# Performance work log

Hardware: AMD Instinct MI355X
Metric: run time of the kernel (lower is better)

The kernel has to match this reference:

```python
import jax, jax.numpy as jnp
import numpy as np

E, T, H, F, G, PACK = 8, 512, 1024, 2816, 128, 8  # experts, tokens, hidden, intermediate, group_size, int4 pack factor


def _pack_int4(nib):
    # nib: [E, K, N] int32 in [0,16) -> packed [E, K//PACK, N] int32 (8 nibbles along K per int32)
    e, k, n = nib.shape
    nib = nib.reshape(e, k // PACK, PACK, n).astype(jnp.uint32)
    shifts = (jnp.arange(PACK, dtype=jnp.uint32) * 4)[None, None, :, None]
    packed = jnp.sum(nib << shifts, axis=2, dtype=jnp.uint32)
    return jax.lax.bitcast_convert_type(packed, jnp.int32)


def _dequant(qw, scales):
    # qw: [E, K//PACK, N] int32, scales: [E, K//G, N] -> [E, K, N] float32, GPTQ sym zero-point 8
    e, kp, n = qw.shape
    k = kp * PACK
    shifts = (jnp.arange(PACK, dtype=jnp.int32) * 4)[None, None, :, None]
    nib = ((qw[:, :, None, :] >> shifts) & 0xF).reshape(e, k, n).astype(jnp.float32) - 8.0
    s = jnp.repeat(scales, G, axis=1)  # [E, K, N]
    return nib * s


def setup_inputs() -> dict:
    key = jax.random.key(0)
    kx, kl, k1, k2, ks1, ks2 = jax.random.split(key, 6)
    x = jax.random.normal(kx, (T, H), dtype=jnp.float32)
    router_logits = jax.random.normal(kl, (T, E), dtype=jnp.float32)
    nib13 = jax.random.randint(k1, (E, H, 2 * F), 0, 16, dtype=jnp.int32)
    nib2 = jax.random.randint(k2, (E, F, H), 0, 16, dtype=jnp.int32)
    w13_qweight = _pack_int4(nib13)   # [E, H//8, 2F]
    w2_qweight = _pack_int4(nib2)     # [E, F//8, H]
    w13_scales = jax.random.uniform(ks1, (E, H // G, 2 * F), dtype=jnp.float32) * 0.02 + 0.001
    w2_scales = jax.random.uniform(ks2, (E, F // G, H), dtype=jnp.float32) * 0.02 + 0.001
    return {"x": x, "router_logits": router_logits, "w13_qweight": w13_qweight,
            "w2_qweight": w2_qweight, "w13_scales": w13_scales, "w2_scales": w2_scales,
            "top_k": 2}


def reference(x, router_logits, w13_qweight, w2_qweight, w13_scales, w2_scales, top_k):
    # --- routing: softmax -> top_k -> renormalize (renormalize=True default) ---
    probs = jax.nn.softmax(router_logits, axis=-1)            # [T, E]
    topk_w, topk_i = jax.lax.top_k(probs, top_k)              # [T, K]
    topk_w = topk_w / jnp.sum(topk_w, axis=-1, keepdims=True)
    # --- dequantize int4 expert weights ---
    W13 = _dequant(w13_qweight, w13_scales)                   # [E, H, 2F]
    W2 = _dequant(w2_qweight, w2_scales)                      # [E, F, H]
    # --- per-expert gated MLP on all tokens, masked combine ---
    h = jnp.einsum('th,ehf->etf', x, W13)                     # [E, T, 2F]
    g, u = h[..., :F], h[..., F:]
    a = jax.nn.silu(g) * u                                    # [E, T, F]
    y = jnp.einsum('etf,efh->eth', a, W2)                     # [E, T, H]
    # combine weights: [T, E], scattering top-k routing weights
    combine = jnp.zeros((x.shape[0], E), dtype=x.dtype).at[
        jnp.arange(x.shape[0])[:, None], topk_i].add(topk_w)
    return jnp.einsum('te,eth->th', combine, y)               # [T, H]
```

## Files before the change

### kernel.cpp

```cpp
#include <hip/hip_runtime.h>
#include <math.h>

#define NE 8
#define NT 512
#define NH 1024
#define NF 2816
#define TWO_F (2*NF)
#define HP (NH/8)
#define FP (NF/8)
#define H_GROUPS 8
#define F_GROUPS 22

typedef __attribute__((ext_vector_type(4))) int   int4v;
typedef __attribute__((ext_vector_type(4))) float f32x4;
typedef __attribute__((ext_vector_type(8))) short short8;

__device__ inline short f2bf(float f) {
    unsigned u = __float_as_uint(f);
    u += 0x7FFFu + ((u >> 16) & 1u);
    return (short)(u >> 16);
}
__device__ inline float bf2f(short s) {
    return __uint_as_float(((unsigned)(unsigned short)s) << 16);
}

__device__ inline void load_lds_16(const void* gsrc, void* ldst) {
    __builtin_amdgcn_global_load_lds(
        (const __attribute__((address_space(1))) unsigned*)gsrc,
        (__attribute__((address_space(3))) unsigned*)ldst, 16, 0, 0);
}

__device__ inline int4v unpack16(int q0, int q1) {
    int e0 = q0 & 0x0F0F0F0F, o0 = ((unsigned)q0 >> 4) & 0x0F0F0F0F;
    int e1 = q1 & 0x0F0F0F0F, o1 = ((unsigned)q1 >> 4) & 0x0F0F0F0F;
    int4v b;
    b[0] = (__builtin_amdgcn_perm(o0, e0, 0x05010400) + 0x78787878) ^ 0x80808080;
    b[1] = (__builtin_amdgcn_perm(o0, e0, 0x07030602) + 0x78787878) ^ 0x80808080;
    b[2] = (__builtin_amdgcn_perm(o1, e1, 0x05010400) + 0x78787878) ^ 0x80808080;
    b[3] = (__builtin_amdgcn_perm(o1, e1, 0x07030602) + 0x78787878) ^ 0x80808080;
    return b;
}

__device__ inline short8 unpack_scale_bf16(int q, float sc) {
    float v[8];
#pragma unroll
    for (int j = 0; j < 8; ++j) {
        unsigned u = 0x4B000000u | (((unsigned)q >> (4 * j)) & 15u);
        v[j] = __uint_as_float(u) - 8388616.0f;
    }
    union { short8 s; unsigned u[4]; } r;
#pragma unroll
    for (int j = 0; j < 4; ++j) {
        unsigned lo = __float_as_uint(v[2 * j] * sc);
        unsigned hi = __float_as_uint(v[2 * j + 1] * sc);
        r.u[j] = __builtin_amdgcn_perm(hi, lo, 0x07060302u);
    }
    return r.s;
}

__device__ inline int pack4(const int* b) {
    return (b[0] & 255) | ((b[1] & 255) << 8) | ((b[2] & 255) << 16) | ((b[3] & 255) << 24);
}

__global__ __launch_bounds__(512) void route_bin_kernel(
        const float* __restrict__ logits,
        float* __restrict__ topk_w,
        int* __restrict__ counts,
        int* __restrict__ offs,
        int* __restrict__ tok_list,
        int* __restrict__ rowmap) {
    __shared__ int sh_e[2 * NT];
    __shared__ int sh_cnt[NE], sh_off[NE];
    const int t = threadIdx.x;
    float l[NE];
#pragma unroll
    for (int e = 0; e < NE; ++e) l[e] = logits[t * NE + e];
    int i0 = 0; float v0 = l[0];
#pragma unroll
    for (int e = 1; e < NE; ++e) { if (l[e] > v0) { v0 = l[e]; i0 = e; } }
    int i1 = -1; float v1 = -INFINITY;
#pragma unroll
    for (int e = 0; e < NE; ++e) {
        if (e == i0) continue;
        if (l[e] > v1) { v1 = l[e]; i1 = e; }
    }
    float e1 = expf(v1 - v0);
    float inv = 1.0f / (1.0f + e1);
    topk_w[t * 2 + 0] = inv;
    topk_w[t * 2 + 1] = e1 * inv;
    sh_e[t * 2 + 0] = i0;
    sh_e[t * 2 + 1] = i1;
    __syncthreads();
    const int w = t >> 6, lane = t & 63;
    int base = 0;
    for (int chunk = 0; chunk < 16; ++chunk) {
        int j = chunk * 64 + lane;
        bool m = (sh_e[j] == w);
        unsigned long long mask = __ballot(m);
        if (m) {
            int pos = base + __popcll(mask & ((1ull << lane) - 1ull));
            tok_list[w * NT + pos] = j;
        }
        base += __popcll(mask);
    }
    if (lane == 0) { counts[w] = base; sh_cnt[w] = base; }
    __syncthreads();
    if (t == 0) {
        int o = 0;
#pragma unroll
        for (int e = 0; e < NE; ++e) { sh_off[e] = o; offs[e] = o; o += sh_cnt[e]; }
    }
    __syncthreads();
    const int myoff = sh_off[w];
    for (int i = lane; i < sh_cnt[w]; i += 64)
        rowmap[myoff + i] = tok_list[w * NT + i];
}

__global__ __launch_bounds__(256) void quant_x_kernel(const float* __restrict__ x,
                                                      const int* __restrict__ rowmap,
                                                      char* __restrict__ xq,
                                                      float* __restrict__ sx) {
    __shared__ float wmax[4];
    const int r = blockIdx.x;
    const int t = rowmap[r] >> 1;
    const int tid = threadIdx.x;
    f32x4 v = *(const f32x4*)(x + (size_t)t * NH + tid * 4);
    float m = fmaxf(fmaxf(fabsf(v[0]), fabsf(v[1])), fmaxf(fabsf(v[2]), fabsf(v[3])));
#pragma unroll
    for (int off = 32; off >= 1; off >>= 1)
        m = fmaxf(m, __shfl_xor(m, off, 64));
    if ((tid & 63) == 0) wmax[tid >> 6] = m;
    __syncthreads();
    float amax = fmaxf(fmaxf(wmax[0], wmax[1]), fmaxf(wmax[2], wmax[3]));
    float scale = (amax > 0.f) ? amax / 127.f : 0.f;
    float invs  = (amax > 0.f) ? 127.f / amax : 0.f;
    if (tid == 0) sx[r] = scale;
    int bq[4];
#pragma unroll
    for (int j = 0; j < 4; ++j) {
        float qh = rintf(v[j] * invs);
        qh = fminf(fmaxf(qh, -127.f), 127.f);
        bq[j] = (int)qh;
    }
    ((int*)xq)[r * (NH / 4) + tid] = pack4(bq);
}

__global__ __launch_bounds__(256) void gemm1_act_kernel(
        const char*  __restrict__ xq,
        const float* __restrict__ sx,
        const int*   __restrict__ w13q,
        const float* __restrict__ s13,
        const int*   __restrict__ counts,
        const int*   __restrict__ offs,
        short* __restrict__ a_s) {
    __shared__ int lds[2][2][16][32];
    const int e = blockIdx.z;
    const int me = counts[e];
    const int mtile = blockIdx.y;
    if (mtile * 64 >= me) return;
    const int base = offs[e];
    const int tid = threadIdx.x;
    const int w = tid >> 6, l = tid & 63;
    const int lr = l & 15, kg = l >> 4;
    const int rb = mtile * 64 + w * 16;
    const int cF0 = blockIdx.x * 32;

    const int sgu  = w >> 1;
    const int srow = (w & 1) * 8 + (l >> 3);
    const int scol = (l & 7) * 4;
    const int* gW = w13q + (size_t)e * HP * TWO_F + (size_t)srow * TWO_F
                  + cF0 + sgu * NF + scol;

    int i = rb + lr; if (i >= me) i = me - 1;
    const char* pA = xq + (size_t)(base + i) * NH;
    const float* sb = s13 + (size_t)e * H_GROUPS * TWO_F + cF0 + lr;

    f32x4 facc[2][2];
#pragma unroll
    for (int gu = 0; gu < 2; ++gu)
#pragma unroll
        for (int ns = 0; ns < 2; ++ns) facc[gu][ns] = (f32x4)0.f;

    load_lds_16(gW, &lds[0][sgu][(w & 1) * 8][0]);
    __syncthreads();
    int buf = 0;
#pragma unroll 1
    for (int kb = 0; kb < H_GROUPS; ++kb) {
        if (kb < H_GROUPS - 1)
            load_lds_16(gW + (size_t)(kb + 1) * 16 * TWO_F,
                        &lds[buf ^ 1][sgu][(w & 1) * 8][0]);
        float scl[2][2];
        scl[0][0] = sb[(size_t)kb * TWO_F];
        scl[0][1] = sb[(size_t)kb * TWO_F + 16];
        scl[1][0] = sb[(size_t)kb * TWO_F + NF];
        scl[1][1] = sb[(size_t)kb * TWO_F + NF + 16];
        int4v ah[2];
#pragma unroll
        for (int ks = 0; ks < 2; ++ks) {
            const int k0 = kb * 128 + ks * 64 + kg * 16;
            ah[ks] = *(const int4v*)(pA + k0);
        }
#pragma unroll
        for (int gu = 0; gu < 2; ++gu)
#pragma unroll
            for (int ns = 0; ns < 2; ++ns) {
                int4v ihh = (int4v)0;
#pragma unroll
                for (int ks = 0; ks < 2; ++ks) {
                    const int row = ks * 8 + kg * 2;
                    const int c = ns * 16 + lr;
                    const int4v b = unpack16(lds[buf][gu][row][c],
                                             lds[buf][gu][row + 1][c]);
                    ihh = __builtin_amdgcn_mfma_i32_16x16x64_i8(ah[ks], b, ihh, 0, 0, 0);
                }
                const float c2 = scl[gu][ns];
#pragma unroll
                for (int r = 0; r < 4; ++r)
                    facc[gu][ns][r] += c2 * (float)ihh[r];
            }
        __syncthreads();
        buf ^= 1;
    }
#pragma unroll
    for (int r = 0; r < 4; ++r) {
        const int orow = rb + kg * 4 + r;
        if (orow < me) {
            const int rg = base + orow;
            const float sxm = sx[rg];
#pragma unroll
            for (int ns = 0; ns < 2; ++ns) {
                const float g = sxm * facc[0][ns][r];
                const float u = sxm * facc[1][ns][r];
                const float aval = (g / (1.0f + __expf(-g))) * u;
                a_s[(size_t)rg * NF + cF0 + ns * 16 + lr] = f2bf(aval);
            }
        }
    }
}

__global__ __launch_bounds__(256) void gemm2_kernel(
        const short* __restrict__ a_s,
        const int*   __restrict__ w2q,
        const float* __restrict__ s2,
        const int*   __restrict__ counts,
        const int*   __restrict__ offs,
        const int*   __restrict__ rowmap,
        const float* __restrict__ topk_w,
        float* __restrict__ out) {
    __shared__ float red[3][32][33];
    const int e = blockIdx.z;
    const int me = counts[e];
    const int mtile = blockIdx.y;
    if (mtile * 32 >= me) return;
    const int base = offs[e];
    const int tid = threadIdx.x;
    const int kh = tid >> 6, l = tid & 63;
    const int lr = l & 15, kg = l >> 4;
    const int rb = mtile * 32;
    const int cb = blockIdx.x * 32;

    const short* aA[2];
#pragma unroll
    for (int ms = 0; ms < 2; ++ms) {
        int i = rb + ms * 16 + lr;
        if (i >= me) i = me - 1;
        aA[ms] = a_s + (size_t)(base + i) * NF;
    }

    f32x4 facc[2][2];
#pragma unroll
    for (int ms = 0; ms < 2; ++ms)
#pragma unroll
        for (int ns = 0; ns < 2; ++ns) facc[ms][ns] = (f32x4)0.f;

    for (int g = kh; g < F_GROUPS; g += 4) {
        float sc[2];
#pragma unroll
        for (int ns = 0; ns < 2; ++ns)
            sc[ns] = s2[(size_t)(e * F_GROUPS + g) * NH + cb + ns * 16 + lr];
#pragma unroll
        for (int ks = 0; ks < 4; ++ks) {
            const int k0 = g * 128 + ks * 32;
            short8 a[2];
#pragma unroll
            for (int ms = 0; ms < 2; ++ms)
                a[ms] = *(const short8*)(aA[ms] + k0 + kg * 8);
            const int kp = (k0 >> 3) + kg;
            const int* bq = w2q + ((size_t)e * FP + kp) * NH + cb + lr;
            int q[2];
#pragma unroll
            for (int ns = 0; ns < 2; ++ns) q[ns] = bq[ns * 16];
#pragma unroll
            for (int ns = 0; ns < 2; ++ns) {
                const short8 b = unpack_scale_bf16(q[ns], sc[ns]);
#pragma unroll
                for (int ms = 0; ms < 2; ++ms)
                    facc[ms][ns] = __builtin_amdgcn_mfma_f32_16x16x32_bf16(a[ms], b, facc[ms][ns], 0, 0, 0);
            }
        }
    }

    if (kh > 0) {
#pragma unroll
        for (int ms = 0; ms < 2; ++ms)
#pragma unroll
            for (int ns = 0; ns < 2; ++ns)
#pragma unroll
                for (int r = 0; r < 4; ++r)
                    red[kh - 1][ms * 16 + kg * 4 + r][ns * 16 + lr] = facc[ms][ns][r];
    }
    __syncthreads();
    if (kh == 0) {
#pragma unroll
        for (int ms = 0; ms < 2; ++ms) {
#pragma unroll
            for (int r = 0; r < 4; ++r) {
                const int rowLoc = ms * 16 + kg * 4 + r;
                const int orow = rb + rowLoc;
                if (orow < me) {
                    const int rg = base + orow;
                    const int t2s = rowmap[rg];
                    const float wscale = topk_w[t2s];
#pragma unroll
                    for (int ns = 0; ns < 2; ++ns) {
                        float v = facc[ms][ns][r]
                                + red[0][rowLoc][ns * 16 + lr]
                                + red[1][rowLoc][ns * 16 + lr]
                                + red[2][rowLoc][ns * 16 + lr];
                        atomicAdd(out + (size_t)(t2s >> 1) * NH + cb + ns * 16 + lr, wscale * v);
                    }
                }
            }
        }
    }
}

extern "C" void kernel_launch(void* const* d_in, const int* in_sizes, int n_in,
                              void* d_out, int out_size, void* d_ws, size_t ws_size,
                              hipStream_t stream) {
    const float* x      = (const float*)d_in[0];
    const float* logits = (const float*)d_in[1];
    const int*   w13q   = (const int*)d_in[2];
    const int*   w2q    = (const int*)d_in[3];
    const float* s13    = (const float*)d_in[4];
    const float* s2     = (const float*)d_in[5];

    char* ws = (char*)d_ws;
    size_t o = 0;
    int*   counts   = (int*)(ws + o);   o += 4096;
    int*   offs     = (int*)(ws + o);   o += 4096;
    float* topk_w   = (float*)(ws + o); o += 4096;
    int*   tok_list = (int*)(ws + o);   o += 16384;
    int*   rowmap   = (int*)(ws + o);   o += 4096;
    float* sx       = (float*)(ws + o); o += 4096;
    char*  xq       = ws + o;           o += (size_t)2 * NT * NH;
    short* a_s      = (short*)(ws + o); o += (size_t)2 * NT * NF * 2;

    hipMemsetAsync(d_out, 0, (size_t)out_size * sizeof(float), stream);
    route_bin_kernel<<<1, 512, 0, stream>>>(logits, topk_w, counts, offs, tok_list, rowmap);
    quant_x_kernel<<<2 * NT, 256, 0, stream>>>(x, rowmap, xq, sx);
    gemm1_act_kernel<<<dim3(NF / 32, 8, NE), 256, 0, stream>>>(
        xq, sx, w13q, s13, counts, offs, a_s);
    gemm2_kernel<<<dim3(NH / 32, 16, NE), 256, 0, stream>>>(
        a_s, w2q, s2, counts, offs, rowmap, topk_w, (float*)d_out);
}
```

Before: 79.99 us.

## Replace atomic scatter and memset with per-row store plus gather combine kernel

The second GEMM now writes unweighted per-(token,slot) results to a workspace buffer instead of doing weighted atomicAdds into the output. A new combine kernel uses an inverse row map built during routing to gather each token's two expert rows, weight them, and write the output directly. This also removes the output memset. The cost is an extra kernel launch and about 4 MB of extra writes and reads through the workspace.

New measurement: 76.91 us. 3.9% less time.

```diff
diff --git a/kernel.cpp b/kernel.cpp
--- a/kernel.cpp
+++ b/kernel.cpp
@@ -68,7 +68,8 @@
         int* __restrict__ counts,
         int* __restrict__ offs,
         int* __restrict__ tok_list,
-        int* __restrict__ rowmap) {
+        int* __restrict__ rowmap,
+        int* __restrict__ inv) {
     __shared__ int sh_e[2 * NT];
     __shared__ int sh_cnt[NE], sh_off[NE];
     const int t = threadIdx.x;
@@ -85,9 +86,9 @@
         if (l[e] > v1) { v1 = l[e]; i1 = e; }
     }
     float e1 = expf(v1 - v0);
-    float inv = 1.0f / (1.0f + e1);
-    topk_w[t * 2 + 0] = inv;
-    topk_w[t * 2 + 1] = e1 * inv;
+    float invp = 1.0f / (1.0f + e1);
+    topk_w[t * 2 + 0] = invp;
+    topk_w[t * 2 + 1] = e1 * invp;
     sh_e[t * 2 + 0] = i0;
     sh_e[t * 2 + 1] = i1;
     __syncthreads();
@@ -112,8 +113,11 @@
     }
     __syncthreads();
     const int myoff = sh_off[w];
-    for (int i = lane; i < sh_cnt[w]; i += 64)
-        rowmap[myoff + i] = tok_list[w * NT + i];
+    for (int i = lane; i < sh_cnt[w]; i += 64) {
+        const int j = tok_list[w * NT + i];
+        rowmap[myoff + i] = j;
+        inv[j] = myoff + i;
+    }
 }
 
 __global__ __launch_bounds__(256) void quant_x_kernel(const float* __restrict__ x,
@@ -244,9 +248,7 @@
         const float* __restrict__ s2,
         const int*   __restrict__ counts,
         const int*   __restrict__ offs,
-        const int*   __restrict__ rowmap,
-        const float* __restrict__ topk_w,
-        float* __restrict__ out) {
+        float* __restrict__ y_s) {
     __shared__ float red[3][32][33];
     const int e = blockIdx.z;
     const int me = counts[e];
@@ -319,20 +321,37 @@
                 const int orow = rb + rowLoc;
                 if (orow < me) {
                     const int rg = base + orow;
-                    const int t2s = rowmap[rg];
-                    const float wscale = topk_w[t2s];
 #pragma unroll
                     for (int ns = 0; ns < 2; ++ns) {
                         float v = facc[ms][ns][r]
                                 + red[0][rowLoc][ns * 16 + lr]
                                 + red[1][rowLoc][ns * 16 + lr]
                                 + red[2][rowLoc][ns * 16 + lr];
-                        atomicAdd(out + (size_t)(t2s >> 1) * NH + cb + ns * 16 + lr, wscale * v);
+                        y_s[(size_t)rg * NH + cb + ns * 16 + lr] = v;
                     }
                 }
             }
         }
     }
+}
+
+__global__ __launch_bounds__(256) void combine_kernel(
+        const float* __restrict__ y_s,
+        const int*   __restrict__ inv,
+        const float* __restrict__ topk_w,
+        float* __restrict__ out) {
+    const int t = blockIdx.x;
+    const int c = threadIdx.x * 4;
+    const float w0 = topk_w[2 * t];
+    const float w1 = topk_w[2 * t + 1];
+    const int r0 = inv[2 * t];
+    const int r1 = inv[2 * t + 1];
+    f32x4 y0 = *(const f32x4*)(y_s + (size_t)r0 * NH + c);
+    f32x4 y1 = *(const f32x4*)(y_s + (size_t)r1 * NH + c);
+    f32x4 o;
+#pragma unroll
+    for (int j = 0; j < 4; ++j) o[j] = w0 * y0[j] + w1 * y1[j];
+    *(f32x4*)(out + (size_t)t * NH + c) = o;
 }
 
 extern "C" void kernel_launch(void* const* d_in, const int* in_sizes, int n_in,
@@ -352,15 +371,18 @@
     float* topk_w   = (float*)(ws + o); o += 4096;
     int*   tok_list = (int*)(ws + o);   o += 16384;
     int*   rowmap   = (int*)(ws + o);   o += 4096;
+    int*   inv      = (int*)(ws + o);   o += 4096;
     float* sx       = (float*)(ws + o); o += 4096;
     char*  xq       = ws + o;           o += (size_t)2 * NT * NH;
     short* a_s      = (short*)(ws + o); o += (size_t)2 * NT * NF * 2;
-
-    hipMemsetAsync(d_out, 0, (size_t)out_size * sizeof(float), stream);
-    route_bin_kernel<<<1, 512, 0, stream>>>(logits, topk_w, counts, offs, tok_list, rowmap);
+    float* y_s      = (float*)(ws + o); o += (size_t)2 * NT * NH * 4;
+
+    route_bin_kernel<<<1, 512, 0, stream>>>(logits, topk_w, counts, offs,
+                                            tok_list, rowmap, inv);
     quant_x_kernel<<<2 * NT, 256, 0, stream>>>(x, rowmap, xq, sx);
     gemm1_act_kernel<<<dim3(NF / 32, 8, NE), 256, 0, stream>>>(
         xq, sx, w13q, s13, counts, offs, a_s);
     gemm2_kernel<<<dim3(NH / 32, 16, NE), 256, 0, stream>>>(
-        a_s, w2q, s2, counts, offs, rowmap, topk_w, (float*)d_out);
-}
+        a_s, w2q, s2, counts, offs, y_s);
+    combine_kernel<<<NT, 256, 0, stream>>>(y_s, inv, topk_w, (float*)d_out);
+}
```
